# Performance work log

Hardware: AMD Instinct MI355X
Metric: run time of the kernel (lower is better)

The kernel has to match this reference:

```python
import jax, jax.numpy as jnp
import numpy as np
import math

B, S, D, H = 2048, 32, 1024, 16
DK = D // H
EPS = 1e-5

def setup_inputs() -> dict:
    key = jax.random.key(0)
    ks = jax.random.split(key, 8)
    w_scale = 0.02  # realistic init scale for linear weights
    # Weights stored as (d_in, d_out): y = x @ W + b (same math as torch x @ W.T)
    return {
        "x":  jax.random.normal(ks[0], (B, S, D), jnp.float32),
        "ln_g": jnp.ones((D,), jnp.float32),
        "ln_b": jnp.zeros((D,), jnp.float32),
        "wq": jax.random.normal(ks[1], (D, D), jnp.float32) * w_scale,
        "bq": jnp.zeros((D,), jnp.float32),
        "wk": jax.random.normal(ks[2], (D, D), jnp.float32) * w_scale,
        "bk": jnp.zeros((D,), jnp.float32),
        "wv": jax.random.normal(ks[3], (D, D), jnp.float32) * w_scale,
        "bv": jnp.zeros((D,), jnp.float32),
        "wo": jax.random.normal(ks[4], (D, D), jnp.float32) * w_scale,
        "bo": jnp.zeros((D,), jnp.float32),
        "rel_bias": jax.random.normal(ks[5], (H, 32, 32), jnp.float32),
    }

def reference(x, ln_g, ln_b, wq, bq, wk, bk, wv, bv, wo, bo, rel_bias):
    b, s, d = x.shape
    h = rel_bias.shape[0]
    dk = d // h
    residual = x
    # LayerNorm (eps=1e-5)
    mu = jnp.mean(x, axis=-1, keepdims=True)
    var = jnp.mean(jnp.square(x - mu), axis=-1, keepdims=True)
    xn = (x - mu) * jax.lax.rsqrt(var + EPS) * ln_g + ln_b
    # QKV projections -> [b, h, s, dk]
    def split_heads(t):
        return t.reshape(b, s, h, dk).transpose(0, 2, 1, 3)
    Q = split_heads(xn @ wq + bq)
    K = split_heads(xn @ wk + bk)
    V = split_heads(xn @ wv + bv)
    scores = jnp.einsum('bhqd,bhkd->bhqk', Q, K) / jnp.sqrt(jnp.float32(dk))
    if s <= 32:  # static at trace time, matching the torch branch
        scores = scores + rel_bias[:, :s, :s][None]
    attn = jax.nn.softmax(scores, axis=-1)
    ctx = jnp.einsum('bhqk,bhkd->bhqd', attn, V)
    ctx = ctx.transpose(0, 2, 1, 3).reshape(b, s, d)
    out = ctx @ wo + bo  # dropout is identity in eval
    return residual + out
```

## Files before the change

### kernel.cpp

```cpp
#include <hip/hip_runtime.h>
#include <stdint.h>


typedef __attribute__((ext_vector_type(8))) short bf16x8;
typedef __attribute__((ext_vector_type(4))) float f32x4;
typedef __attribute__((ext_vector_type(16))) float f32x16;

__device__ __forceinline__ float bf2f(unsigned short u) {
    return __uint_as_float(((unsigned)u) << 16);
}
__device__ __forceinline__ unsigned short f2bf(float f) {
    unsigned u = __float_as_uint(f);
    u += 0x7FFFu + ((u >> 16) & 1u);
    return (unsigned short)(u >> 16);
}
__device__ __forceinline__ uint4 pack8(const float* f) {
    uint4 u;
    u.x = (unsigned)f2bf(f[0]) | ((unsigned)f2bf(f[1]) << 16);
    u.y = (unsigned)f2bf(f[2]) | ((unsigned)f2bf(f[3]) << 16);
    u.z = (unsigned)f2bf(f[4]) | ((unsigned)f2bf(f[5]) << 16);
    u.w = (unsigned)f2bf(f[6]) | ((unsigned)f2bf(f[7]) << 16);
    return u;
}

typedef __attribute__((address_space(3))) unsigned lds_u32;
typedef const __attribute__((address_space(1))) unsigned glb_u32;
__device__ __forceinline__ void gld16(const void* g, void* l) {
    __builtin_amdgcn_global_load_lds((glb_u32*)g, (lds_u32*)l, 16, 0, 0);
}

__global__ __launch_bounds__(256) void lnw_kernel(
    const float* __restrict__ x, const float* __restrict__ gg,
    const float* __restrict__ bb, unsigned short* __restrict__ xn,
    const float* __restrict__ wq, const float* __restrict__ wk,
    const float* __restrict__ wv, const float* __restrict__ wo,
    unsigned short* __restrict__ wcatT, unsigned short* __restrict__ woT)
{
    __shared__ unsigned short T[64 * 72];
    if (blockIdx.x >= 8192) {
        int bid = blockIdx.x - 8192;
        int p = bid >> 8;
        int t = bid & 255;
        int k0 = (t >> 4) * 64, n0 = (t & 15) * 64;
        const float* src = (p == 0) ? wq : (p == 1) ? wk : (p == 2) ? wv : wo;
        unsigned short* dst = (p < 3) ? (wcatT + (size_t)p * 1048576) : woT;
        int tid = threadIdx.x;
#pragma unroll
        for (int it = 0; it < 2; it++) {
            int flat = it * 2048 + tid * 8;
            int r = flat >> 6, c = flat & 63;
            const float* s4 = src + (size_t)(k0 + r) * 1024 + n0 + c;
            float4 u0 = *(const float4*)s4;
            float4 u1 = *(const float4*)(s4 + 4);
            float f[8] = {u0.x, u0.y, u0.z, u0.w, u1.x, u1.y, u1.z, u1.w};
            *(uint4*)&T[r * 72 + c] = pack8(f);
        }
        __syncthreads();
#pragma unroll
        for (int it = 0; it < 2; it++) {
            int flat = it * 2048 + tid * 8;
            int rn = flat >> 6, ck = flat & 63;
            unsigned short v[8];
#pragma unroll
            for (int j = 0; j < 8; j++) v[j] = T[(ck + j) * 72 + rn];
            uint4 u;
            u.x = (unsigned)v[0] | ((unsigned)v[1] << 16);
            u.y = (unsigned)v[2] | ((unsigned)v[3] << 16);
            u.z = (unsigned)v[4] | ((unsigned)v[5] << 16);
            u.w = (unsigned)v[6] | ((unsigned)v[7] << 16);
            *(uint4*)(dst + (size_t)(n0 + rn) * 1024 + k0 + ck) = u;
        }
        return;
    }
    int l = threadIdx.x & 63;
    float fg0[8], fg1[8], fb0[8], fb1[8];
    *(float4*)&fg0[0] = *(const float4*)(gg + l * 8);
    *(float4*)&fg0[4] = *(const float4*)(gg + l * 8 + 4);
    *(float4*)&fg1[0] = *(const float4*)(gg + 512 + l * 8);
    *(float4*)&fg1[4] = *(const float4*)(gg + 512 + l * 8 + 4);
    *(float4*)&fb0[0] = *(const float4*)(bb + l * 8);
    *(float4*)&fb0[4] = *(const float4*)(bb + l * 8 + 4);
    *(float4*)&fb1[0] = *(const float4*)(bb + 512 + l * 8);
    *(float4*)&fb1[4] = *(const float4*)(bb + 512 + l * 8 + 4);
#pragma unroll
    for (int rr = 0; rr < 2; rr++) {
        size_t row = (size_t)blockIdx.x * 8 + (threadIdx.x >> 6) * 2 + rr;
        const float* xr = x + row * 1024;
        float f0[8], f1[8];
        *(float4*)&f0[0] = *(const float4*)(xr + l * 8);
        *(float4*)&f0[4] = *(const float4*)(xr + l * 8 + 4);
        *(float4*)&f1[0] = *(const float4*)(xr + 512 + l * 8);
        *(float4*)&f1[4] = *(const float4*)(xr + 512 + l * 8 + 4);
        float s = 0.f, s2 = 0.f;
#pragma unroll
        for (int j = 0; j < 8; j++) { s += f0[j] + f1[j]; s2 += f0[j] * f0[j] + f1[j] * f1[j]; }
#pragma unroll
        for (int m = 1; m < 64; m <<= 1) { s += __shfl_xor(s, m); s2 += __shfl_xor(s2, m); }
        float mu = s * (1.f / 1024.f);
        float var = s2 * (1.f / 1024.f) - mu * mu;
        float rs = rsqrtf(var + 1e-5f);
        float o0[8], o1[8];
#pragma unroll
        for (int j = 0; j < 8; j++) {
            o0[j] = (f0[j] - mu) * rs * fg0[j] + fb0[j];
            o1[j] = (f1[j] - mu) * rs * fg1[j] + fb1[j];
        }
        *(uint4*)(xn + row * 1024 + l * 8) = pack8(o0);
        *(uint4*)(xn + row * 1024 + 512 + l * 8) = pack8(o1);
    }
}

#define FENCE asm volatile("" ::: "memory")
#define BARRIER do { FENCE; __builtin_amdgcn_s_barrier(); FENCE; } while (0)
#define WAIT_LGKM0 do { asm volatile("s_waitcnt lgkmcnt(0)" ::: "memory"); \
                        __builtin_amdgcn_sched_barrier(0); } while (0)
#define VMCNT(n) asm volatile("s_waitcnt vmcnt(" #n ")" ::: "memory")

#define FQ_SA(buf) (LDSU + (buf) * 8192)
#define FQ_SB(buf) (LDSU + 16384 + (buf) * 12288)
#define QS_OFF 0
#define KS_OFF 9216
#define VT_OFF 18432
#define PS_OFF 28672

#define ASTG(buf, g, koff) gld16(Ag + (size_t)(g) * 32768 + (koff), \
                                 FQ_SA(buf) + ((g) * 32 + w * 8) * 64)
#define BSTG(buf, p, c, koff) gld16(((p) == 0 ? Bgq : (p) == 1 ? Bgk : Bgv) + (size_t)(c) * 32768 + (koff), \
                                    FQ_SB(buf) + ((p) * 64 + (c) * 32 + w * 8) * 64)

#define FLDA(buf, q, ks) (*(const bf16x8*)&FQ_SA(buf)[ \
    (wm * 64 + (q) * 16 + (l & 15)) * 64 + ((((ks) * 32) + khi) ^ aswz)])
#define FLDB(buf, cf, ks) (*(const bf16x8*)&FQ_SB(buf)[ \
    (wn * 96 + (cf) * 16 + (l & 15)) * 64 + ((((ks) * 32) + khi) ^ aswz)])

#define MFMA_HEX2(q, a0, a1) do { \
    _Pragma("unroll") \
    for (int cf = 0; cf < 6; cf++) { \
        acc[q][cf] = __builtin_amdgcn_mfma_f32_16x16x32_bf16(a0, bF[cf][0], acc[q][cf], 0, 0, 0); \
        acc[q][cf] = __builtin_amdgcn_mfma_f32_16x16x32_bf16(a1, bF[cf][1], acc[q][cf], 0, 0, 0); \
    } } while (0)

#define FPHASE2(buf, q0, LOADB, STAGE_STMT, TAIL_STMT) do { \
    bf16x8 aF0 = FLDA(buf, q0, 0), aF1 = FLDA(buf, q0, 1); \
    bf16x8 aG0 = FLDA(buf, (q0) + 1, 0), aG1 = FLDA(buf, (q0) + 1, 1); \
    if (LOADB) { \
        _Pragma("unroll") \
        for (int cf = 0; cf < 6; cf++) { bF[cf][0] = FLDB(buf, cf, 0); bF[cf][1] = FLDB(buf, cf, 1); } \
    } \
    STAGE_STMT; \
    BARRIER; \
    WAIT_LGKM0; \
    __builtin_amdgcn_s_setprio(1); \
    MFMA_HEX2(q0, aF0, aF1); \
    MFMA_HEX2((q0) + 1, aG0, aG1); \
    __builtin_amdgcn_s_setprio(0); \
    TAIL_STMT; \
    BARRIER; \
} while (0)

__global__ __launch_bounds__(256, 2) void fqa2_kernel(
    const unsigned short* __restrict__ A, const unsigned short* __restrict__ wcatT,
    const float* __restrict__ bq, const float* __restrict__ bk,
    const float* __restrict__ bv, const float* __restrict__ rb,
    unsigned short* __restrict__ ctx)
{
    __shared__ __align__(16) unsigned short LDSU[40960];
    int bx = blockIdx.x;
    int h  = ((bx & 7) << 1) | ((bx >> 3) & 1);
    int mp = bx >> 4;
    int m0 = mp * 128;
    int tid = threadIdx.x, l = tid & 63, w = tid >> 6;
    int wm = w >> 1, wn = w & 1;
    int khi = (l >> 4) * 8;
    int aswz = (l & 7) * 8;
    int swzc = ((l & 7) ^ (l >> 3)) * 8;

    const unsigned short* Ag  = A + (size_t)(m0 + w * 8 + (l >> 3)) * 1024 + swzc;
    const unsigned short* Bgq = wcatT + (size_t)(h * 64 + w * 8 + (l >> 3)) * 1024 + swzc;
    const unsigned short* Bgk = Bgq + 1048576ull;
    const unsigned short* Bgv = Bgq + 2097152ull;

    f32x4 acc[4][6];
#pragma unroll
    for (int i = 0; i < 4; i++)
#pragma unroll
        for (int j = 0; j < 6; j++)
#pragma unroll
            for (int v = 0; v < 4; v++) acc[i][j][v] = 0.f;

    bf16x8 bF[6][2];

    ASTG(0, 0, 0); ASTG(0, 1, 0); ASTG(0, 2, 0); ASTG(0, 3, 0);
    BSTG(0, 0, 0, 0); BSTG(0, 0, 1, 0); BSTG(0, 1, 0, 0);
    BSTG(0, 1, 1, 0); BSTG(0, 2, 0, 0); BSTG(0, 2, 1, 0);
    BSTG(1, 0, 0, 64); BSTG(1, 0, 1, 64); BSTG(1, 1, 0, 64);
    BSTG(1, 1, 1, 64); BSTG(1, 2, 0, 64); BSTG(1, 2, 1, 64);
    VMCNT(6);
    BARRIER;

    for (int it = 0; it < 7; ++it) {
        int ko1 = (2 * it + 1) * 64, ko2 = (2 * it + 2) * 64, ko3 = (2 * it + 3) * 64;
        FPHASE2(0, 0, 1,
            do { ASTG(1, 0, ko1); ASTG(1, 1, ko1); ASTG(1, 2, ko1); ASTG(1, 3, ko1); } while (0),
            (void)0);
        FPHASE2(0, 2, 0,
            do { BSTG(0, 0, 0, ko2); BSTG(0, 0, 1, ko2); BSTG(0, 1, 0, ko2);
                 BSTG(0, 1, 1, ko2); BSTG(0, 2, 0, ko2); BSTG(0, 2, 1, ko2); } while (0),
            VMCNT(6));
        FPHASE2(1, 0, 1,
            do { ASTG(0, 0, ko2); ASTG(0, 1, ko2); ASTG(0, 2, ko2); ASTG(0, 3, ko2); } while (0),
            (void)0);
        FPHASE2(1, 2, 0,
            do { BSTG(1, 0, 0, ko3); BSTG(1, 0, 1, ko3); BSTG(1, 1, 0, ko3);
                 BSTG(1, 1, 1, ko3); BSTG(1, 2, 0, ko3); BSTG(1, 2, 1, ko3); } while (0),
            VMCNT(6));
    }
    FPHASE2(0, 0, 1,
        do { ASTG(1, 0, 960); ASTG(1, 1, 960); ASTG(1, 2, 960); ASTG(1, 3, 960); } while (0),
        (void)0);
    FPHASE2(0, 2, 0, (void)0, VMCNT(0));
    FPHASE2(1, 0, 1, (void)0, (void)0);
    FPHASE2(1, 2, 0, (void)0, (void)0);
    __builtin_amdgcn_sched_barrier(0);

#pragma unroll
    for (int cf = 0; cf < 6; cf++) {
        int colg = wn * 96 + cf * 16 + (l & 15);
        int seg = colg >> 6;
        int cseg = colg & 63;
        const float* bp = (seg == 0) ? bq : (seg == 1) ? bk : bv;
        float bias = bp[h * 64 + cseg];
#pragma unroll
        for (int ai = 0; ai < 4; ai++) {
#pragma unroll
            for (int v = 0; v < 4; v++) {
                int row = wm * 64 + ai * 16 + (l >> 4) * 4 + v;
                unsigned short val = f2bf(acc[ai][cf][v] + bias);
                if (seg == 0)      LDSU[QS_OFF + row * 72 + cseg] = val;
                else if (seg == 1) LDSU[KS_OFF + row * 72 + cseg] = val;
                else               LDSU[VT_OFF + (((row >> 5) << 6) + cseg) * 40 + (row & 31)] = val;
            }
        }
    }
    __syncthreads();

    {
        int col = l & 31, hi = l >> 5;
        f32x16 s;
#pragma unroll
        for (int i = 0; i < 16; i++) s[i] = 0.f;
#pragma unroll
        for (int t = 0; t < 4; t++) {
            bf16x8 aQ = *(const bf16x8*)&LDSU[QS_OFF + (w * 32 + col) * 72 + t * 16 + hi * 8];
            bf16x8 bK = *(const bf16x8*)&LDSU[KS_OFF + (w * 32 + col) * 72 + t * 16 + hi * 8];
            s = __builtin_amdgcn_mfma_f32_32x32x16_bf16(aQ, bK, s, 0, 0, 0);
        }
        const float* rbh = rb + h * 1024;
        unsigned short* ps = LDSU + PS_OFF + w * 1280;
#pragma unroll
        for (int r = 0; r < 16; r++) {
            int m = (r & 3) + 8 * (r >> 2) + 4 * hi;
            float v = s[r] * 0.125f + rbh[m * 32 + col];
            float e = __expf(v);
            float sm = e;
#pragma unroll
            for (int msk = 1; msk < 32; msk <<= 1) sm += __shfl_xor(sm, msk);
            float rinv;
            asm("v_rcp_f32 %0, %1" : "=v"(rinv) : "v"(sm));
            rinv = rinv * (2.0f - sm * rinv);
            ps[m * 40 + col] = f2bf(e * rinv);
        }
        unsigned short* vtw = LDSU + VT_OFF + w * 2560;
        bf16x8 pa0 = *(const bf16x8*)&ps[col * 40 + hi * 8];
        bf16x8 pa1 = *(const bf16x8*)&ps[col * 40 + 16 + hi * 8];
        bf16x8 vb00 = *(const bf16x8*)&vtw[(col) * 40 + hi * 8];
        bf16x8 vb01 = *(const bf16x8*)&vtw[(col) * 40 + 16 + hi * 8];
        bf16x8 vb10 = *(const bf16x8*)&vtw[(32 + col) * 40 + hi * 8];
        bf16x8 vb11 = *(const bf16x8*)&vtw[(32 + col) * 40 + 16 + hi * 8];
        f32x16 o0, o1;
#pragma unroll
        for (int i = 0; i < 16; i++) { o0[i] = 0.f; o1[i] = 0.f; }
        o0 = __builtin_amdgcn_mfma_f32_32x32x16_bf16(pa0, vb00, o0, 0, 0, 0);
        o0 = __builtin_amdgcn_mfma_f32_32x32x16_bf16(pa1, vb01, o0, 0, 0, 0);
        o1 = __builtin_amdgcn_mfma_f32_32x32x16_bf16(pa0, vb10, o1, 0, 0, 0);
        o1 = __builtin_amdgcn_mfma_f32_32x32x16_bf16(pa1, vb11, o1, 0, 0, 0);

#pragma unroll
        for (int r = 0; r < 16; r++) {
            int m = (r & 3) + 8 * (r >> 2) + 4 * hi;
            vtw[m * 72 + col]      = f2bf(o0[r]);
            vtw[m * 72 + 32 + col] = f2bf(o1[r]);
        }
        size_t rowb = ((size_t)mp * 4 + w) * 32;
#pragma unroll
        for (int pass = 0; pass < 4; pass++) {
            int row = pass * 8 + (l >> 3);
            int c = (l & 7) * 8;
            uint4 val = *(const uint4*)&vtw[row * 72 + c];
            *(uint4*)(ctx + (rowb + row) * 1024 + h * 64 + c) = val;
        }
    }
}

#define SAp(buf) (LDSB + (buf) * 16384)
#define SBp(buf) (LDSB + 32768 + (buf) * 16384)

#define STG(gb, hh, kcol, ldsreg) do { \
    const unsigned short* _g = (gb) + (size_t)((hh) * 128) * 1024 + (kcol); \
    unsigned short* _d = (ldsreg) + ((hh) * 128 + w * 8) * 64; \
    gld16(_g, _d); gld16(_g + 64 * 1024, _d + 64 * 64); } while (0)

#define LDA(buf, q, rfq, ks) (*(const bf16x8*)&SAp(buf)[ \
    (wm * 128 + (q) * 32 + (rfq) * 16 + (l & 15)) * 64 + ((((ks) * 32) + khi) ^ aswz)])
#define LDB(buf, cf, ks) (*(const bf16x8*)&SBp(buf)[ \
    (wn * 64 + (cf) * 16 + (l & 15)) * 64 + ((((ks) * 32) + khi) ^ aswz)])

#define MFMA_QUAD(q) do { \
    _Pragma("unroll") \
    for (int cf = 0; cf < 4; cf++) { \
        acc[(q)*2+0][cf] = __builtin_amdgcn_mfma_f32_16x16x32_bf16(aF00, bF[cf][0], acc[(q)*2+0][cf], 0, 0, 0); \
        acc[(q)*2+0][cf] = __builtin_amdgcn_mfma_f32_16x16x32_bf16(aF01, bF[cf][1], acc[(q)*2+0][cf], 0, 0, 0); \
        acc[(q)*2+1][cf] = __builtin_amdgcn_mfma_f32_16x16x32_bf16(aF10, bF[cf][0], acc[(q)*2+1][cf], 0, 0, 0); \
        acc[(q)*2+1][cf] = __builtin_amdgcn_mfma_f32_16x16x32_bf16(aF11, bF[cf][1], acc[(q)*2+1][cf], 0, 0, 0); \
    } } while (0)

#define PHASE(buf, q, STAGE_STMT, TAIL_STMT) do { \
    bf16x8 aF00 = LDA(buf, q, 0, 0), aF01 = LDA(buf, q, 0, 1); \
    bf16x8 aF10 = LDA(buf, q, 1, 0), aF11 = LDA(buf, q, 1, 1); \
    if ((q) == 0) { \
        _Pragma("unroll") \
        for (int cf = 0; cf < 4; cf++) { bF[cf][0] = LDB(buf, cf, 0); bF[cf][1] = LDB(buf, cf, 1); } \
    } \
    STAGE_STMT; \
    BARRIER; \
    WAIT_LGKM0; \
    __builtin_amdgcn_s_setprio(1); \
    MFMA_QUAD(q); \
    __builtin_amdgcn_s_setprio(0); \
    TAIL_STMT; \
    BARRIER; \
} while (0)

__global__ __launch_bounds__(512, 2) void gemm8res(
    const unsigned short* __restrict__ A, const unsigned short* __restrict__ Bt,
    const float* __restrict__ bz0, const float* __restrict__ resid,
    float* __restrict__ out, int NTL)
{
    __shared__ __align__(16) unsigned short LDSB[65536];
    int cpx = gridDim.x >> 3;
    int bid = (blockIdx.x & 7) * cpx + (blockIdx.x >> 3);
    int mt = bid / NTL, ntl = bid % NTL;
    int m0 = mt * 256, n0 = ntl * 256;
    int tid = threadIdx.x, l = tid & 63, w = tid >> 6;
    int wm = w >> 2, wn = w & 3;
    int khi = (l >> 4) * 8;
    int aswz = (l & 7) * 8;

    const unsigned short* Ag = A + (size_t)(m0 + w * 8 + (l >> 3)) * 1024 + ((l & 7) ^ (l >> 3)) * 8;
    const unsigned short* Bg = Bt + (size_t)(n0 + w * 8 + (l >> 3)) * 1024 + ((l & 7) ^ (l >> 3)) * 8;
    unsigned short* sA0 = SAp(0);
    unsigned short* sA1 = SAp(1);
    unsigned short* sB0 = SBp(0);
    unsigned short* sB1 = SBp(1);

    f32x4 acc[8][4];
#pragma unroll
    for (int i = 0; i < 8; i++)
#pragma unroll
        for (int j = 0; j < 4; j++)
#pragma unroll
            for (int v = 0; v < 4; v++) acc[i][j][v] = 0.f;

    bf16x8 bF[4][2];

    STG(Ag, 0, 0, sA0); STG(Ag, 1, 0, sA0);
    STG(Bg, 0, 0, sB0); STG(Bg, 1, 0, sB0);
    STG(Bg, 0, 64, sB1); STG(Bg, 1, 64, sB1);
    VMCNT(4);
    BARRIER;

    for (int it = 0; it < 7; ++it) {
        int koff = it * 128;
        PHASE(0, 0, STG(Ag, 0, koff + 64, sA1), (void)0);
        PHASE(0, 1, STG(Ag, 1, koff + 64, sA1), (void)0);
        PHASE(0, 2, STG(Bg, 0, koff + 128, sB0), (void)0);
        PHASE(0, 3, STG(Bg, 1, koff + 128, sB0), VMCNT(4));
        PHASE(1, 0, STG(Ag, 0, koff + 128, sA0), (void)0);
        PHASE(1, 1, STG(Ag, 1, koff + 128, sA0), (void)0);
        PHASE(1, 2, STG(Bg, 0, koff + 192, sB1), (void)0);
        PHASE(1, 3, STG(Bg, 1, koff + 192, sB1), VMCNT(4));
    }
    PHASE(0, 0, STG(Ag, 0, 960, sA1), (void)0);
    PHASE(0, 1, STG(Ag, 1, 960, sA1), (void)0);
    PHASE(0, 2, (void)0, (void)0);
    PHASE(0, 3, (void)0, VMCNT(0));
    PHASE(1, 0, (void)0, (void)0);
    PHASE(1, 1, (void)0, (void)0);
    PHASE(1, 2, (void)0, (void)0);
    PHASE(1, 3, (void)0, (void)0);
    __builtin_amdgcn_sched_barrier(0);

    float* Cf = (float*)LDSB;
    int gcol = n0 + l * 4;
    float4 bzv = *(const float4*)(bz0 + gcol);
#pragma unroll
    for (int pass = 0; pass < 2; pass++) {
        __syncthreads();
#pragma unroll
        for (int rfq = 0; rfq < 4; rfq++) {
            int rf = pass * 4 + rfq;
#pragma unroll
            for (int cf = 0; cf < 4; cf++) {
                int c0 = wn * 64 + cf * 16 + (l & 15);
                int c4 = c0 >> 2, ce = c0 & 3;
#pragma unroll
                for (int v = 0; v < 4; v++) {
                    int rl = wm * 64 + rfq * 16 + (l >> 4) * 4 + v;
                    Cf[rl * 256 + ((c4 ^ (rl & 7)) << 2) + ce] = acc[rf][cf][v];
                }
            }
        }
        __syncthreads();
#pragma unroll
        for (int rb4 = 0; rb4 < 4; rb4++) {
            float4 rz[4], cv[4];
#pragma unroll
            for (int k = 0; k < 4; k++) {
                int rr = (rb4 * 4 + k) * 8 + w;
                int grow = m0 + (rr & 63) + ((rr >> 6) << 7) + pass * 64;
                rz[k] = *(const float4*)(resid + (size_t)grow * 1024 + gcol);
            }
#pragma unroll
            for (int k = 0; k < 4; k++) {
                int rr = (rb4 * 4 + k) * 8 + w;
                cv[k] = *(const float4*)&Cf[rr * 256 + ((l ^ (rr & 7)) << 2)];
            }
#pragma unroll
            for (int k = 0; k < 4; k++) {
                int rr = (rb4 * 4 + k) * 8 + w;
                int grow = m0 + (rr & 63) + ((rr >> 6) << 7) + pass * 64;
                float4 o;
                o.x = cv[k].x + bzv.x + rz[k].x;
                o.y = cv[k].y + bzv.y + rz[k].y;
                o.z = cv[k].z + bzv.z + rz[k].z;
                o.w = cv[k].w + bzv.w + rz[k].w;
                *(float4*)(out + (size_t)grow * 1024 + gcol) = o;
            }
        }
    }
}

extern "C" void kernel_launch(void* const* d_in, const int* in_sizes, int n_in,
                              void* d_out, int out_size, void* d_ws, size_t ws_size,
                              hipStream_t stream)
{
    const float* x  = (const float*)d_in[0];
    const float* lg = (const float*)d_in[1];
    const float* lb = (const float*)d_in[2];
    const float* wq = (const float*)d_in[3];
    const float* bq = (const float*)d_in[4];
    const float* wk = (const float*)d_in[5];
    const float* bk = (const float*)d_in[6];
    const float* wv = (const float*)d_in[7];
    const float* bv = (const float*)d_in[8];
    const float* wo = (const float*)d_in[9];
    const float* bo = (const float*)d_in[10];
    const float* rb = (const float*)d_in[11];
    float* out = (float*)d_out;
    unsigned short* ws = (unsigned short*)d_ws;

    unsigned short* wcatT = ws;
    unsigned short* woT   = wcatT + 3145728;
    unsigned short* xn    = woT + 1048576;
    unsigned short* ctx   = xn + 67108864ull;

    lnw_kernel<<<dim3(9216), dim3(256), 0, stream>>>(
        x, lg, lb, xn, wq, wk, wv, wo, wcatT, woT);

    fqa2_kernel<<<dim3(8192), dim3(256), 0, stream>>>(xn, wcatT, bq, bk, bv, rb, ctx);

    gemm8res<<<dim3(1024), dim3(512), 0, stream>>>(ctx, woT, bo, x, out, 4);
}
```

Baseline: 719.9 us.

## Double fused QKV-attention block to 512 threads, halving per-warp accumulator tiles

The fused QKV projection plus attention kernel now runs 8 waves per block instead of 4, each wave owning 32 rows instead of 64 of the 128-row tile, so accumulators and A-fragment loads halve. Staging loads are split across twice as many threads, and the attention epilogue assigns two waves per 32-row batch, each computing half of the output columns. An extra block barrier is added before the context write. This is meant to raise occupancy and cut register pressure, at the cost of more B-fragment LDS reads per MFMA and more barrier participants.

```diff
diff --git a/kernel.cpp b/kernel.cpp
--- a/kernel.cpp
+++ b/kernel.cpp
@@ -123,26 +123,25 @@
 #define VT_OFF 18432
 #define PS_OFF 28672
 
-#define ASTG(buf, g, koff) gld16(Ag + (size_t)(g) * 32768 + (koff), \
-                                 FQ_SA(buf) + ((g) * 32 + w * 8) * 64)
-#define BSTG(buf, p, c, koff) gld16(((p) == 0 ? Bgq : (p) == 1 ? Bgk : Bgv) + (size_t)(c) * 32768 + (koff), \
-                                    FQ_SB(buf) + ((p) * 64 + (c) * 32 + w * 8) * 64)
+#define ASTG(buf, g, koff) gld16(Ag + (size_t)(g) * 65536 + (koff), \
+                                 FQ_SA(buf) + ((g) * 64 + w * 8) * 64)
+#define BSTG(buf, c, koff) gld16(((c) == 0 ? Bgq : (c) == 1 ? Bgk : Bgv) + (koff), \
+                                 FQ_SB(buf) + ((c) * 64 + w * 8) * 64)
 
 #define FLDA(buf, q, ks) (*(const bf16x8*)&FQ_SA(buf)[ \
-    (wm * 64 + (q) * 16 + (l & 15)) * 64 + ((((ks) * 32) + khi) ^ aswz)])
+    (wm * 32 + (q) * 16 + (l & 15)) * 64 + ((((ks) * 32) + khi) ^ aswz)])
 #define FLDB(buf, cf, ks) (*(const bf16x8*)&FQ_SB(buf)[ \
     (wn * 96 + (cf) * 16 + (l & 15)) * 64 + ((((ks) * 32) + khi) ^ aswz)])
 
-#define MFMA_HEX2(q, a0, a1) do { \
+#define MFMA_DOZ(q, a0, a1) do { \
     _Pragma("unroll") \
     for (int cf = 0; cf < 6; cf++) { \
         acc[q][cf] = __builtin_amdgcn_mfma_f32_16x16x32_bf16(a0, bF[cf][0], acc[q][cf], 0, 0, 0); \
         acc[q][cf] = __builtin_amdgcn_mfma_f32_16x16x32_bf16(a1, bF[cf][1], acc[q][cf], 0, 0, 0); \
     } } while (0)
 
-#define FPHASE2(buf, q0, LOADB, STAGE_STMT, TAIL_STMT) do { \
-    bf16x8 aF0 = FLDA(buf, q0, 0), aF1 = FLDA(buf, q0, 1); \
-    bf16x8 aG0 = FLDA(buf, (q0) + 1, 0), aG1 = FLDA(buf, (q0) + 1, 1); \
+#define FPHASE(buf, q, LOADB, STAGE_STMT, TAIL_STMT) do { \
+    bf16x8 aF0 = FLDA(buf, q, 0), aF1 = FLDA(buf, q, 1); \
     if (LOADB) { \
         _Pragma("unroll") \
         for (int cf = 0; cf < 6; cf++) { bF[cf][0] = FLDB(buf, cf, 0); bF[cf][1] = FLDB(buf, cf, 1); } \
@@ -151,14 +150,13 @@
     BARRIER; \
     WAIT_LGKM0; \
     __builtin_amdgcn_s_setprio(1); \
-    MFMA_HEX2(q0, aF0, aF1); \
-    MFMA_HEX2((q0) + 1, aG0, aG1); \
+    MFMA_DOZ(q, aF0, aF1); \
     __builtin_amdgcn_s_setprio(0); \
     TAIL_STMT; \
     BARRIER; \
 } while (0)
 
-__global__ __launch_bounds__(256, 2) void fqa2_kernel(
+__global__ __launch_bounds__(512, 2) void fqa3_kernel(
     const unsigned short* __restrict__ A, const unsigned short* __restrict__ wcatT,
     const float* __restrict__ bq, const float* __restrict__ bk,
     const float* __restrict__ bv, const float* __restrict__ rb,
@@ -180,9 +178,9 @@
     const unsigned short* Bgk = Bgq + 1048576ull;
     const unsigned short* Bgv = Bgq + 2097152ull;
 
-    f32x4 acc[4][6];
-#pragma unroll
-    for (int i = 0; i < 4; i++)
+    f32x4 acc[2][6];
+#pragma unroll
+    for (int i = 0; i < 2; i++)
 #pragma unroll
         for (int j = 0; j < 6; j++)
 #pragma unroll
@@ -190,37 +188,23 @@
 
     bf16x8 bF[6][2];
 
-    ASTG(0, 0, 0); ASTG(0, 1, 0); ASTG(0, 2, 0); ASTG(0, 3, 0);
-    BSTG(0, 0, 0, 0); BSTG(0, 0, 1, 0); BSTG(0, 1, 0, 0);
-    BSTG(0, 1, 1, 0); BSTG(0, 2, 0, 0); BSTG(0, 2, 1, 0);
-    BSTG(1, 0, 0, 64); BSTG(1, 0, 1, 64); BSTG(1, 1, 0, 64);
-    BSTG(1, 1, 1, 64); BSTG(1, 2, 0, 64); BSTG(1, 2, 1, 64);
-    VMCNT(6);
+    ASTG(0, 0, 0); ASTG(0, 1, 0);
+    BSTG(0, 0, 0); BSTG(0, 1, 0); BSTG(0, 2, 0);
+    BSTG(1, 0, 64); BSTG(1, 1, 64); BSTG(1, 2, 64);
+    VMCNT(3);
     BARRIER;
 
     for (int it = 0; it < 7; ++it) {
         int ko1 = (2 * it + 1) * 64, ko2 = (2 * it + 2) * 64, ko3 = (2 * it + 3) * 64;
-        FPHASE2(0, 0, 1,
-            do { ASTG(1, 0, ko1); ASTG(1, 1, ko1); ASTG(1, 2, ko1); ASTG(1, 3, ko1); } while (0),
-            (void)0);
-        FPHASE2(0, 2, 0,
-            do { BSTG(0, 0, 0, ko2); BSTG(0, 0, 1, ko2); BSTG(0, 1, 0, ko2);
-                 BSTG(0, 1, 1, ko2); BSTG(0, 2, 0, ko2); BSTG(0, 2, 1, ko2); } while (0),
-            VMCNT(6));
-        FPHASE2(1, 0, 1,
-            do { ASTG(0, 0, ko2); ASTG(0, 1, ko2); ASTG(0, 2, ko2); ASTG(0, 3, ko2); } while (0),
-            (void)0);
-        FPHASE2(1, 2, 0,
-            do { BSTG(1, 0, 0, ko3); BSTG(1, 0, 1, ko3); BSTG(1, 1, 0, ko3);
-                 BSTG(1, 1, 1, ko3); BSTG(1, 2, 0, ko3); BSTG(1, 2, 1, ko3); } while (0),
-            VMCNT(6));
-    }
-    FPHASE2(0, 0, 1,
-        do { ASTG(1, 0, 960); ASTG(1, 1, 960); ASTG(1, 2, 960); ASTG(1, 3, 960); } while (0),
-        (void)0);
-    FPHASE2(0, 2, 0, (void)0, VMCNT(0));
-    FPHASE2(1, 0, 1, (void)0, (void)0);
-    FPHASE2(1, 2, 0, (void)0, (void)0);
+        FPHASE(0, 0, 1, do { ASTG(1, 0, ko1); ASTG(1, 1, ko1); } while (0), (void)0);
+        FPHASE(0, 1, 0, do { BSTG(0, 0, ko2); BSTG(0, 1, ko2); BSTG(0, 2, ko2); } while (0), VMCNT(3));
+        FPHASE(1, 0, 1, do { ASTG(0, 0, ko2); ASTG(0, 1, ko2); } while (0), (void)0);
+        FPHASE(1, 1, 0, do { BSTG(1, 0, ko3); BSTG(1, 1, ko3); BSTG(1, 2, ko3); } while (0), VMCNT(3));
+    }
+    FPHASE(0, 0, 1, do { ASTG(1, 0, 960); ASTG(1, 1, 960); } while (0), (void)0);
+    FPHASE(0, 1, 0, (void)0, VMCNT(0));
+    FPHASE(1, 0, 1, (void)0, (void)0);
+    FPHASE(1, 1, 0, (void)0, (void)0);
     __builtin_amdgcn_sched_barrier(0);
 
 #pragma unroll
@@ -231,11 +215,11 @@
         const float* bp = (seg == 0) ? bq : (seg == 1) ? bk : bv;
         float bias = bp[h * 64 + cseg];
 #pragma unroll
-        for (int ai = 0; ai < 4; ai++) {
+        for (int q = 0; q < 2; q++) {
 #pragma unroll
             for (int v = 0; v < 4; v++) {
-                int row = wm * 64 + ai * 16 + (l >> 4) * 4 + v;
-                unsigned short val = f2bf(acc[ai][cf][v] + bias);
+                int row = wm * 32 + q * 16 + (l >> 4) * 4 + v;
+                unsigned short val = f2bf(acc[q][cf][v] + bias);
                 if (seg == 0)      LDSU[QS_OFF + row * 72 + cseg] = val;
                 else if (seg == 1) LDSU[KS_OFF + row * 72 + cseg] = val;
                 else               LDSU[VT_OFF + (((row >> 5) << 6) + cseg) * 40 + (row & 31)] = val;
@@ -245,18 +229,19 @@
     __syncthreads();
 
     {
+        int b4 = w >> 1, c2 = w & 1;
         int col = l & 31, hi = l >> 5;
         f32x16 s;
 #pragma unroll
         for (int i = 0; i < 16; i++) s[i] = 0.f;
 #pragma unroll
         for (int t = 0; t < 4; t++) {
-            bf16x8 aQ = *(const bf16x8*)&LDSU[QS_OFF + (w * 32 + col) * 72 + t * 16 + hi * 8];
-            bf16x8 bK = *(const bf16x8*)&LDSU[KS_OFF + (w * 32 + col) * 72 + t * 16 + hi * 8];
+            bf16x8 aQ = *(const bf16x8*)&LDSU[QS_OFF + (b4 * 32 + col) * 72 + t * 16 + hi * 8];
+            bf16x8 bK = *(const bf16x8*)&LDSU[KS_OFF + (b4 * 32 + col) * 72 + t * 16 + hi * 8];
             s = __builtin_amdgcn_mfma_f32_32x32x16_bf16(aQ, bK, s, 0, 0, 0);
         }
         const float* rbh = rb + h * 1024;
-        unsigned short* ps = LDSU + PS_OFF + w * 1280;
+        unsigned short* ps = LDSU + PS_OFF + b4 * 1280;
 #pragma unroll
         for (int r = 0; r < 16; r++) {
             int m = (r & 3) + 8 * (r >> 2) + 4 * hi;
@@ -270,32 +255,29 @@
             rinv = rinv * (2.0f - sm * rinv);
             ps[m * 40 + col] = f2bf(e * rinv);
         }
-        unsigned short* vtw = LDSU + VT_OFF + w * 2560;
+        unsigned short* vtw = LDSU + VT_OFF + b4 * 2560;
         bf16x8 pa0 = *(const bf16x8*)&ps[col * 40 + hi * 8];
         bf16x8 pa1 = *(const bf16x8*)&ps[col * 40 + 16 + hi * 8];
-        bf16x8 vb00 = *(const bf16x8*)&vtw[(col) * 40 + hi * 8];
-        bf16x8 vb01 = *(const bf16x8*)&vtw[(col) * 40 + 16 + hi * 8];
-        bf16x8 vb10 = *(const bf16x8*)&vtw[(32 + col) * 40 + hi * 8];
-        bf16x8 vb11 = *(const bf16x8*)&vtw[(32 + col) * 40 + 16 + hi * 8];
-        f32x16 o0, o1;
-#pragma unroll
-        for (int i = 0; i < 16; i++) { o0[i] = 0.f; o1[i] = 0.f; }
-        o0 = __builtin_amdgcn_mfma_f32_32x32x16_bf16(pa0, vb00, o0, 0, 0, 0);
-        o0 = __builtin_amdgcn_mfma_f32_32x32x16_bf16(pa1, vb01, o0, 0, 0, 0);
-        o1 = __builtin_amdgcn_mfma_f32_32x32x16_bf16(pa0, vb10, o1, 0, 0, 0);
-        o1 = __builtin_amdgcn_mfma_f32_32x32x16_bf16(pa1, vb11, o1, 0, 0, 0);
+        bf16x8 vb0 = *(const bf16x8*)&vtw[(c2 * 32 + col) * 40 + hi * 8];
+        bf16x8 vb1 = *(const bf16x8*)&vtw[(c2 * 32 + col) * 40 + 16 + hi * 8];
+        f32x16 o;
+#pragma unroll
+        for (int i = 0; i < 16; i++) o[i] = 0.f;
+        o = __builtin_amdgcn_mfma_f32_32x32x16_bf16(pa0, vb0, o, 0, 0, 0);
+        o = __builtin_amdgcn_mfma_f32_32x32x16_bf16(pa1, vb1, o, 0, 0, 0);
+
+        __syncthreads();
 
 #pragma unroll
         for (int r = 0; r < 16; r++) {
             int m = (r & 3) + 8 * (r >> 2) + 4 * hi;
-            vtw[m * 72 + col]      = f2bf(o0[r]);
-            vtw[m * 72 + 32 + col] = f2bf(o1[r]);
-        }
-        size_t rowb = ((size_t)mp * 4 + w) * 32;
-#pragma unroll
-        for (int pass = 0; pass < 4; pass++) {
-            int row = pass * 8 + (l >> 3);
-            int c = (l & 7) * 8;
+            vtw[m * 72 + c2 * 32 + col] = f2bf(o[r]);
+        }
+        size_t rowb = ((size_t)mp * 4 + b4) * 32;
+#pragma unroll
+        for (int pass = 0; pass < 2; pass++) {
+            int row = pass * 16 + (l >> 2);
+            int c = c2 * 32 + (l & 3) * 8;
             uint4 val = *(const uint4*)&vtw[row * 72 + c];
             *(uint4*)(ctx + (rowb + row) * 1024 + h * 64 + c) = val;
         }
@@ -477,7 +459,7 @@
     lnw_kernel<<<dim3(9216), dim3(256), 0, stream>>>(
         x, lg, lb, xn, wq, wk, wv, wo, wcatT, woT);
 
-    fqa2_kernel<<<dim3(8192), dim3(256), 0, stream>>>(xn, wcatT, bq, bk, bv, rb, ctx);
+    fqa3_kernel<<<dim3(8192), dim3(512), 0, stream>>>(xn, wcatT, bq, bk, bv, rb, ctx);
 
     gemm8res<<<dim3(1024), dim3(512), 0, stream>>>(ctx, woT, bo, x, out, 4);
 }
```

New measurement: 883.3 us. +22.7%, slower.
